# Kernel optimization log

Hardware: AMD Instinct MI355X
Metric: run time of the kernel (lower is better)

## Reference

```python
import jax, jax.numpy as jnp
import numpy as np

N_NODES = 50000
N_EDGES = 800000
IN_DIM, HID_DIM, OUT_DIM = 64, 128, 64


def gcn_conv(x, src, dst, W, b, n_nodes):
    # PyG GCNConv default: add self-loops, symmetric normalization D^-1/2 A D^-1/2
    h = x @ W  # [N, F_out]
    ones = jnp.ones(src.shape[0], dtype=x.dtype)
    deg = jax.ops.segment_sum(ones, dst, num_segments=n_nodes)  # in-degree incl. self-loops
    dinv = jnp.where(deg > 0, jax.lax.rsqrt(deg), 0.0).astype(x.dtype)
    norm = dinv[src] * dinv[dst]  # [E]
    msg = h[src] * norm[:, None]  # gather + scale, [E, F_out]
    out = jax.ops.segment_sum(msg, dst, num_segments=n_nodes)  # scatter-add
    return out + b


def setup_inputs() -> dict:
    key = jax.random.key(0)
    k1, k2, k3, k4 = jax.random.split(key, 4)
    z = jax.random.normal(k1, (N_NODES, IN_DIM), dtype=jnp.float32)
    edge_index = jax.random.randint(k2, (2, N_EDGES), 0, N_NODES, dtype=jnp.int64)
    # Glorot-style init for weights, zero bias (PyG defaults)
    W1 = jax.random.normal(k3, (IN_DIM, HID_DIM), dtype=jnp.float32) / np.sqrt(IN_DIM)
    b1 = jnp.zeros((HID_DIM,), dtype=jnp.float32)
    W2 = jax.random.normal(k4, (HID_DIM, OUT_DIM), dtype=jnp.float32) / np.sqrt(HID_DIM)
    b2 = jnp.zeros((OUT_DIM,), dtype=jnp.float32)
    return {"z": z, "edge_index": edge_index, "W1": W1, "b1": b1, "W2": W2, "b2": b2}


def reference(z, edge_index, W1, b1, W2, b2):
    n = z.shape[0]
    loops = jnp.arange(n, dtype=edge_index.dtype)
    src = jnp.concatenate([edge_index[0], loops])
    dst = jnp.concatenate([edge_index[1], loops])
    h = jax.nn.relu(gcn_conv(z, src, dst, W1, b1, n))
    x_hat = gcn_conv(h, src, dst, W2, b2, n)
    return x_hat
```

## Files before the change

### kernel.cpp

```cpp
#include <hip/hip_runtime.h>
#include <hip/hip_bf16.h>

#define N_NODES 50000
#define N_EDGES 800000
#define IN_DIM 64
#define HID_DIM 128
#define OUT_DIM 64
#define NGRP 8
#define NE8 (NGRP * N_NODES)
#define NBLK8 ((NE8 + 255) / 256)
#define MAXE 128

__device__ int g_in_f32;
__device__ int g_is64;
__device__ int g_src[N_EDGES];
__device__ int g_dst[N_EDGES];
__device__ int g_csr[N_EDGES];
__device__ int g_deg8[NE8];
__device__ int g_rowptr8[NE8 + 1];
__device__ int g_cursor8[NE8];
__device__ int g_bsum[NBLK8];
__device__ int g_boff[NBLK8];
__device__ float g_dinv[N_NODES];
__device__ __align__(16) float g_W1f[IN_DIM * HID_DIM];
__device__ __align__(16) float g_W2f[HID_DIM * OUT_DIM];
__device__ __align__(16) float g_b1f[HID_DIM];
__device__ __align__(16) float g_b2f[OUT_DIM];
__device__ __align__(16) float g_hs1[(size_t)N_NODES * HID_DIM];
__device__ __align__(16) float g_agg1[(size_t)N_NODES * HID_DIM];

__device__ __forceinline__ float loadx(const void* p, int i, int f32) {
    if (f32) return ((const float*)p)[i];
    unsigned int u = ((unsigned int)((const unsigned short*)p)[i]) << 16;
    return __uint_as_float(u);
}

__global__ void detect_kernel(const unsigned short* __restrict__ zw,
                              const unsigned int* __restrict__ ew, int E) {
    __shared__ int s_f32, s_nz;
    if (threadIdx.x == 0) { s_f32 = 0; s_nz = 0; }
    __syncthreads();
    int hit = 0;
    for (int k = 0; k < 64; k++) {
        int i = 2 * ((threadIdx.x * 64 + k) * 97);
        if (((zw[i] >> 7) & 0xFF) == 0xFF) hit = 1;
    }
    if (hit) atomicOr(&s_f32, 1);
    int nz = 0;
    int step = E / 4096;
    for (int k = 0; k < 4; k++) {
        int idx = 1 + 2 * ((threadIdx.x * 4 + k) * step);
        if (ew[idx] != 0) nz = 1;
    }
    if (nz) atomicOr(&s_nz, 1);
    __syncthreads();
    if (threadIdx.x == 0) { g_in_f32 = s_f32; g_is64 = (s_nz == 0) ? 1 : 0; }
}

__global__ void prep_kernel(const void* __restrict__ W1, const void* __restrict__ b1,
                            const void* __restrict__ W2, const void* __restrict__ b2) {
    int i = blockIdx.x * blockDim.x + threadIdx.x;
    if (i < NE8) g_deg8[i] = 0;
    int f32 = g_in_f32;
    if (i < IN_DIM * HID_DIM) g_W1f[i] = loadx(W1, i, f32);
    if (i < HID_DIM * OUT_DIM) g_W2f[i] = loadx(W2, i, f32);
    if (i < HID_DIM) g_b1f[i] = loadx(b1, i, f32);
    if (i < OUT_DIM) g_b2f[i] = loadx(b2, i, f32);
}

__global__ void convert_kernel(const void* __restrict__ ei, int N, int E) {
    int e = blockIdx.x * blockDim.x + threadIdx.x;
    if (e < E) {
        int s, d;
        if (g_is64) {
            const long long* p = (const long long*)ei;
            s = (int)p[e];
            d = (int)p[E + e];
        } else {
            const int* p = (const int*)ei;
            s = p[e];
            d = p[E + e];
        }
        g_src[e] = s;
        g_dst[e] = d;
        int g = blockIdx.x & (NGRP - 1);
        atomicAdd(&g_deg8[g * N + d], 1);
    }
}

__global__ void dinv_kernel(int N) {
    int v = blockIdx.x * blockDim.x + threadIdx.x;
    if (v < N) {
        int s = 0;
#pragma unroll
        for (int g = 0; g < NGRP; g++) s += g_deg8[g * N + v];
        g_dinv[v] = rsqrtf((float)s + 1.0f);
    }
}

__global__ __launch_bounds__(256) void localscan_kernel(int NE) {
    __shared__ int sc[256];
    int t = threadIdx.x;
    int idx = blockIdx.x * 256 + t;
    int d = (idx < NE) ? g_deg8[idx] : 0;
    sc[t] = d;
    __syncthreads();
    for (int off = 1; off < 256; off <<= 1) {
        int v = (t >= off) ? sc[t - off] : 0;
        __syncthreads();
        sc[t] += v;
        __syncthreads();
    }
    if (idx < NE) g_rowptr8[idx] = sc[t] - d;
    if (t == 255) g_bsum[blockIdx.x] = sc[255];
}

__global__ __launch_bounds__(256) void bscan_kernel(int NB, int NE, int E) {
    __shared__ int sc[256];
    int t = threadIdx.x;
    int loc[8];
    int s = 0;
#pragma unroll
    for (int j = 0; j < 8; j++) {
        int i = t * 8 + j;
        int v = (i < NB) ? g_bsum[i] : 0;
        loc[j] = s;
        s += v;
    }
    sc[t] = s;
    __syncthreads();
    for (int off = 1; off < 256; off <<= 1) {
        int v = (t >= off) ? sc[t - off] : 0;
        __syncthreads();
        sc[t] += v;
        __syncthreads();
    }
    int excl = sc[t] - s;
#pragma unroll
    for (int j = 0; j < 8; j++) {
        int i = t * 8 + j;
        if (i < NB) g_boff[i] = excl + loc[j];
    }
    if (t == 0) g_rowptr8[NE] = E;
}

__global__ __launch_bounds__(256) void addoff_kernel(int NE) {
    int idx = blockIdx.x * 256 + threadIdx.x;
    if (idx < NE) {
        int base = g_rowptr8[idx] + g_boff[blockIdx.x];
        g_rowptr8[idx] = base;
        g_cursor8[idx] = base;
    }
}

__global__ void scatter_kernel(int N, int E) {
    int e = blockIdx.x * blockDim.x + threadIdx.x;
    if (e < E) {
        int g = blockIdx.x & (NGRP - 1);
        int pos = atomicAdd(&g_cursor8[g * N + g_dst[e]], 1);
        g_csr[pos] = g_src[e];
    }
}

__global__ __launch_bounds__(256) void aggz_kernel(const void* __restrict__ z, int N) {
    __shared__ int idxbuf[4][MAXE];
    int wid = (blockIdx.x * blockDim.x + threadIdx.x) >> 6;
    if (wid >= N) return;
    int lane = threadIdx.x & 63;
    int w = threadIdx.x >> 6;
    int f32 = g_in_f32;
    int mybeg = 0, mycnt = 0;
    if (lane < NGRP) {
        mybeg = g_rowptr8[lane * N + wid];
        mycnt = g_rowptr8[lane * N + wid + 1] - mybeg;
    }
    int incl = mycnt;
#pragma unroll
    for (int off = 1; off < NGRP; off <<= 1) {
        int v = __shfl_up(incl, off, 64);
        if (lane >= off) incl += v;
    }
    int total = __shfl(incl, NGRP - 1, 64);
    int myoff = incl - mycnt;
    int* buf = idxbuf[w];
    float a0 = loadx(z, wid * IN_DIM + lane, f32) * g_dinv[wid];
    float a1 = 0.f, a2 = 0.f, a3 = 0.f, a4 = 0.f, a5 = 0.f, a6 = 0.f, a7 = 0.f;
    if (total <= MAXE) {
        if (lane < NGRP) {
            for (int i = 0; i < mycnt; i++) buf[myoff + i] = g_csr[mybeg + i];
        }
        int j = 0;
        for (; j + 8 <= total; j += 8) {
            int i0 = buf[j], i1 = buf[j+1], i2 = buf[j+2], i3 = buf[j+3];
            int i4 = buf[j+4], i5 = buf[j+5], i6 = buf[j+6], i7 = buf[j+7];
            a0 += loadx(z, i0 * IN_DIM + lane, f32) * g_dinv[i0];
            a1 += loadx(z, i1 * IN_DIM + lane, f32) * g_dinv[i1];
            a2 += loadx(z, i2 * IN_DIM + lane, f32) * g_dinv[i2];
            a3 += loadx(z, i3 * IN_DIM + lane, f32) * g_dinv[i3];
            a4 += loadx(z, i4 * IN_DIM + lane, f32) * g_dinv[i4];
            a5 += loadx(z, i5 * IN_DIM + lane, f32) * g_dinv[i5];
            a6 += loadx(z, i6 * IN_DIM + lane, f32) * g_dinv[i6];
            a7 += loadx(z, i7 * IN_DIM + lane, f32) * g_dinv[i7];
        }
        if (j + 4 <= total) {
            int i0 = buf[j], i1 = buf[j+1], i2 = buf[j+2], i3 = buf[j+3];
            a0 += loadx(z, i0 * IN_DIM + lane, f32) * g_dinv[i0];
            a1 += loadx(z, i1 * IN_DIM + lane, f32) * g_dinv[i1];
            a2 += loadx(z, i2 * IN_DIM + lane, f32) * g_dinv[i2];
            a3 += loadx(z, i3 * IN_DIM + lane, f32) * g_dinv[i3];
            j += 4;
        }
        for (; j < total; j++) {
            int i0 = buf[j];
            a0 += loadx(z, i0 * IN_DIM + lane, f32) * g_dinv[i0];
        }
    } else {
        for (int g = 0; g < NGRP; g++) {
            int beg = g_rowptr8[g * N + wid], end = g_rowptr8[g * N + wid + 1];
            for (int e = beg; e < end; e++) {
                int s = g_csr[e];
                a0 += loadx(z, s * IN_DIM + lane, f32) * g_dinv[s];
            }
        }
    }
    float acc = ((a0 + a1) + (a2 + a3)) + ((a4 + a5) + (a6 + a7));
    g_hs1[(size_t)wid * 64 + lane] = acc * g_dinv[wid];
}

__global__ __launch_bounds__(256) void gemm1_kernel(int N) {
    __shared__ float Zs[IN_DIM * 33];
    int t = threadIdx.x;
    int row0 = blockIdx.x * 32;
    const float* aggz = g_hs1;
#pragma unroll
    for (int s = 0; s < 2; s++) {
        int i = t + s * 256;
        int r = i >> 4, k4 = i & 15;
        int row = row0 + r;
        float4 v = make_float4(0.f, 0.f, 0.f, 0.f);
        if (row < N) v = *(const float4*)&aggz[(size_t)row * IN_DIM + k4 * 4];
        Zs[(k4 * 4 + 0) * 33 + r] = v.x;
        Zs[(k4 * 4 + 1) * 33 + r] = v.y;
        Zs[(k4 * 4 + 2) * 33 + r] = v.z;
        Zs[(k4 * 4 + 3) * 33 + r] = v.w;
    }
    __syncthreads();
    int cg = t & 31, rg = t >> 5;
    int c0 = cg * 4, r0 = rg * 4;
    float acc[4][4] = {};
#pragma unroll 8
    for (int k = 0; k < IN_DIM; k++) {
        float b[4];
        *(float4*)b = *(const float4*)&g_W1f[k * HID_DIM + c0];
        float a[4];
        a[0] = Zs[k * 33 + r0];
        a[1] = Zs[k * 33 + r0 + 1];
        a[2] = Zs[k * 33 + r0 + 2];
        a[3] = Zs[k * 33 + r0 + 3];
#pragma unroll
        for (int i = 0; i < 4; i++)
#pragma unroll
            for (int j = 0; j < 4; j++) acc[i][j] = fmaf(a[i], b[j], acc[i][j]);
    }
    float4 bias = *(const float4*)&g_b1f[c0];
#pragma unroll
    for (int i = 0; i < 4; i++) {
        int row = row0 + r0 + i;
        if (row < N) {
            float4 v;
            v.x = fmaxf(acc[i][0] + bias.x, 0.f);
            v.y = fmaxf(acc[i][1] + bias.y, 0.f);
            v.z = fmaxf(acc[i][2] + bias.z, 0.f);
            v.w = fmaxf(acc[i][3] + bias.w, 0.f);
            *(float4*)&g_agg1[(size_t)row * HID_DIM + c0] = v;
        }
    }
}

__global__ __launch_bounds__(256) void gemm2_kernel(int N) {
    __shared__ float Zs[64 * 33];
    int t = threadIdx.x;
    int row0 = blockIdx.x * 32;
    int cg = t & 15, rg = t >> 4;
    int c0 = cg * 4, r0 = rg * 2;
    float acc[2][4] = {};
    for (int kh = 0; kh < 2; kh++) {
        __syncthreads();
#pragma unroll
        for (int s = 0; s < 2; s++) {
            int i = t + s * 256;
            int r = i >> 4, k4 = i & 15;
            int row = row0 + r;
            float4 v = make_float4(0.f, 0.f, 0.f, 0.f);
            if (row < N) v = *(const float4*)&g_agg1[(size_t)row * HID_DIM + kh * 64 + k4 * 4];
            Zs[(k4 * 4 + 0) * 33 + r] = v.x;
            Zs[(k4 * 4 + 1) * 33 + r] = v.y;
            Zs[(k4 * 4 + 2) * 33 + r] = v.z;
            Zs[(k4 * 4 + 3) * 33 + r] = v.w;
        }
        __syncthreads();
#pragma unroll 8
        for (int k2 = 0; k2 < 64; k2++) {
            float b[4];
            *(float4*)b = *(const float4*)&g_W2f[(kh * 64 + k2) * OUT_DIM + c0];
            float a[2];
            a[0] = Zs[k2 * 33 + r0];
            a[1] = Zs[k2 * 33 + r0 + 1];
#pragma unroll
            for (int i = 0; i < 2; i++)
#pragma unroll
                for (int j = 0; j < 4; j++) acc[i][j] = fmaf(a[i], b[j], acc[i][j]);
        }
    }
#pragma unroll
    for (int i = 0; i < 2; i++) {
        int row = row0 + r0 + i;
        if (row < N) {
            float dn = g_dinv[row];
            float4 v;
            v.x = acc[i][0] * dn;
            v.y = acc[i][1] * dn;
            v.z = acc[i][2] * dn;
            v.w = acc[i][3] * dn;
            *(float4*)&g_hs1[(size_t)row * OUT_DIM + c0] = v;
        }
    }
}

__global__ __launch_bounds__(256) void agg2_kernel(void* __restrict__ out, int N) {
    __shared__ int idxbuf[4][MAXE];
    int wid = (blockIdx.x * blockDim.x + threadIdx.x) >> 6;
    if (wid >= N) return;
    int lane = threadIdx.x & 63;
    int w = threadIdx.x >> 6;
    const float* hs = g_hs1;
    int mybeg = 0, mycnt = 0;
    if (lane < NGRP) {
        mybeg = g_rowptr8[lane * N + wid];
        mycnt = g_rowptr8[lane * N + wid + 1] - mybeg;
    }
    int incl = mycnt;
#pragma unroll
    for (int off = 1; off < NGRP; off <<= 1) {
        int v = __shfl_up(incl, off, 64);
        if (lane >= off) incl += v;
    }
    int total = __shfl(incl, NGRP - 1, 64);
    int myoff = incl - mycnt;
    int* buf = idxbuf[w];
    float a0 = hs[(size_t)wid * 64 + lane];
    float a1 = 0.f, a2 = 0.f, a3 = 0.f, a4 = 0.f, a5 = 0.f, a6 = 0.f, a7 = 0.f;
    if (total <= MAXE) {
        if (lane < NGRP) {
            for (int i = 0; i < mycnt; i++) buf[myoff + i] = g_csr[mybeg + i];
        }
        int j = 0;
        for (; j + 8 <= total; j += 8) {
            int i0 = buf[j], i1 = buf[j+1], i2 = buf[j+2], i3 = buf[j+3];
            int i4 = buf[j+4], i5 = buf[j+5], i6 = buf[j+6], i7 = buf[j+7];
            a0 += hs[(size_t)i0 * 64 + lane];
            a1 += hs[(size_t)i1 * 64 + lane];
            a2 += hs[(size_t)i2 * 64 + lane];
            a3 += hs[(size_t)i3 * 64 + lane];
            a4 += hs[(size_t)i4 * 64 + lane];
            a5 += hs[(size_t)i5 * 64 + lane];
            a6 += hs[(size_t)i6 * 64 + lane];
            a7 += hs[(size_t)i7 * 64 + lane];
        }
        if (j + 4 <= total) {
            int i0 = buf[j], i1 = buf[j+1], i2 = buf[j+2], i3 = buf[j+3];
            a0 += hs[(size_t)i0 * 64 + lane];
            a1 += hs[(size_t)i1 * 64 + lane];
            a2 += hs[(size_t)i2 * 64 + lane];
            a3 += hs[(size_t)i3 * 64 + lane];
            j += 4;
        }
        for (; j < total; j++) a0 += hs[(size_t)buf[j] * 64 + lane];
    } else {
        for (int g = 0; g < NGRP; g++) {
            int beg = g_rowptr8[g * N + wid], end = g_rowptr8[g * N + wid + 1];
            for (int e = beg; e < end; e++) a0 += hs[(size_t)g_csr[e] * 64 + lane];
        }
    }
    float acc = ((a0 + a1) + (a2 + a3)) + ((a4 + a5) + (a6 + a7));
    float v = acc * g_dinv[wid] + g_b2f[lane];
    if (g_in_f32) ((float*)out)[(size_t)wid * 64 + lane] = v;
    else ((__hip_bfloat16*)out)[(size_t)wid * 64 + lane] = __float2bfloat16(v);
}

extern "C" void kernel_launch(void* const* d_in, const int* in_sizes, int n_in,
                              void* d_out, int out_size, void* d_ws, size_t ws_size,
                              hipStream_t stream) {
    const void* z  = d_in[0];
    const void* ei = d_in[1];
    const void* W1 = d_in[2];
    const void* b1 = d_in[3];
    const void* W2 = d_in[4];
    const void* b2 = d_in[5];

    const int N = in_sizes[0] / IN_DIM;
    const int E = in_sizes[1] / 2;
    const int NE = NGRP * N;

    detect_kernel<<<1, 256, 0, stream>>>((const unsigned short*)z, (const unsigned int*)ei, E);
    prep_kernel<<<NBLK8, 256, 0, stream>>>(W1, b1, W2, b2);
    convert_kernel<<<(E + 255) / 256, 256, 0, stream>>>(ei, N, E);
    dinv_kernel<<<(N + 255) / 256, 256, 0, stream>>>(N);
    localscan_kernel<<<(NE + 255) / 256, 256, 0, stream>>>(NE);
    bscan_kernel<<<1, 256, 0, stream>>>((NE + 255) / 256, NE, E);
    addoff_kernel<<<(NE + 255) / 256, 256, 0, stream>>>(NE);
    scatter_kernel<<<(E + 255) / 256, 256, 0, stream>>>(N, E);

    aggz_kernel<<<(N * 64 + 255) / 256, 256, 0, stream>>>(z, N);
    gemm1_kernel<<<(N + 31) / 32, 256, 0, stream>>>(N);
    gemm2_kernel<<<(N + 31) / 32, 256, 0, stream>>>(N);
    agg2_kernel<<<(N * 64 + 255) / 256, 256, 0, stream>>>(d_out, N);
}
```

Measured before the change: 322.3 us.

## Split feature matrices into 8-column slices for cache-friendly gather aggregation

Features are stored in eight column slices (one 32-byte chunk per node per slice), and each aggregation block now processes one slice. A wavefront handles one node, with 8 lanes per edge and 8 edges in flight, followed by a shuffle reduction. The idea is that each slice (about 1.6 MB) stays resident in cache while the random neighbour gathers run, at the cost of 8x more index-list reads and scans. A z pre-scaling kernel is added, and the GEMM loads and stores are remapped to the sliced layout.

After: 515.7 us. 60.0% more time.

```diff
diff --git a/kernel.cpp b/kernel.cpp
--- a/kernel.cpp
+++ b/kernel.cpp
@@ -9,7 +9,7 @@
 #define NGRP 8
 #define NE8 (NGRP * N_NODES)
 #define NBLK8 ((NE8 + 255) / 256)
-#define MAXE 128
+#define MAXE 256
 
 __device__ int g_in_f32;
 __device__ int g_is64;
@@ -162,13 +162,18 @@
     }
 }
 
-__global__ __launch_bounds__(256) void aggz_kernel(const void* __restrict__ z, int N) {
-    __shared__ int idxbuf[4][MAXE];
-    int wid = (blockIdx.x * blockDim.x + threadIdx.x) >> 6;
-    if (wid >= N) return;
-    int lane = threadIdx.x & 63;
-    int w = threadIdx.x >> 6;
-    int f32 = g_in_f32;
+__global__ void zprep_kernel(const void* __restrict__ z, int N) {
+    int i = blockIdx.x * blockDim.x + threadIdx.x;
+    if (i < N * IN_DIM) {
+        int node = i >> 6, c = i & 63;
+        int g = c >> 3, off = c & 7;
+        g_agg1[(size_t)g * (N * 8) + node * 8 + off] = loadx(z, i, g_in_f32) * g_dinv[node];
+    }
+}
+
+template <int SELF_SCALED>
+__device__ __forceinline__ void agg_slice(const float* __restrict__ slice, float* __restrict__ dst,
+                                          int wid, int g, int lane, int* buf, int N) {
     int mybeg = 0, mycnt = 0;
     if (lane < NGRP) {
         mybeg = g_rowptr8[lane * N + wid];
@@ -182,67 +187,67 @@
     }
     int total = __shfl(incl, NGRP - 1, 64);
     int myoff = incl - mycnt;
-    int* buf = idxbuf[w];
-    float a0 = loadx(z, wid * IN_DIM + lane, f32) * g_dinv[wid];
-    float a1 = 0.f, a2 = 0.f, a3 = 0.f, a4 = 0.f, a5 = 0.f, a6 = 0.f, a7 = 0.f;
+    int col = lane & 7;
+    int eslot = lane >> 3;
+    float acc = 0.f, acc2 = 0.f;
     if (total <= MAXE) {
         if (lane < NGRP) {
             for (int i = 0; i < mycnt; i++) buf[myoff + i] = g_csr[mybeg + i];
         }
-        int j = 0;
-        for (; j + 8 <= total; j += 8) {
-            int i0 = buf[j], i1 = buf[j+1], i2 = buf[j+2], i3 = buf[j+3];
-            int i4 = buf[j+4], i5 = buf[j+5], i6 = buf[j+6], i7 = buf[j+7];
-            a0 += loadx(z, i0 * IN_DIM + lane, f32) * g_dinv[i0];
-            a1 += loadx(z, i1 * IN_DIM + lane, f32) * g_dinv[i1];
-            a2 += loadx(z, i2 * IN_DIM + lane, f32) * g_dinv[i2];
-            a3 += loadx(z, i3 * IN_DIM + lane, f32) * g_dinv[i3];
-            a4 += loadx(z, i4 * IN_DIM + lane, f32) * g_dinv[i4];
-            a5 += loadx(z, i5 * IN_DIM + lane, f32) * g_dinv[i5];
-            a6 += loadx(z, i6 * IN_DIM + lane, f32) * g_dinv[i6];
-            a7 += loadx(z, i7 * IN_DIM + lane, f32) * g_dinv[i7];
-        }
-        if (j + 4 <= total) {
-            int i0 = buf[j], i1 = buf[j+1], i2 = buf[j+2], i3 = buf[j+3];
-            a0 += loadx(z, i0 * IN_DIM + lane, f32) * g_dinv[i0];
-            a1 += loadx(z, i1 * IN_DIM + lane, f32) * g_dinv[i1];
-            a2 += loadx(z, i2 * IN_DIM + lane, f32) * g_dinv[i2];
-            a3 += loadx(z, i3 * IN_DIM + lane, f32) * g_dinv[i3];
-            j += 4;
-        }
-        for (; j < total; j++) {
-            int i0 = buf[j];
-            a0 += loadx(z, i0 * IN_DIM + lane, f32) * g_dinv[i0];
-        }
+        int j = eslot;
+        for (; j + 8 < total; j += 16) {
+            int s0 = buf[j], s1 = buf[j + 8];
+            acc += slice[s0 * 8 + col];
+            acc2 += slice[s1 * 8 + col];
+        }
+        if (j < total) acc += slice[buf[j] * 8 + col];
     } else {
-        for (int g = 0; g < NGRP; g++) {
-            int beg = g_rowptr8[g * N + wid], end = g_rowptr8[g * N + wid + 1];
+        for (int gg = 0; gg < NGRP; gg++) {
+            int beg = g_rowptr8[gg * N + wid], end = g_rowptr8[gg * N + wid + 1];
             for (int e = beg; e < end; e++) {
                 int s = g_csr[e];
-                a0 += loadx(z, s * IN_DIM + lane, f32) * g_dinv[s];
+                if (lane < 8) acc += slice[s * 8 + col];
             }
         }
     }
-    float acc = ((a0 + a1) + (a2 + a3)) + ((a4 + a5) + (a6 + a7));
-    g_hs1[(size_t)wid * 64 + lane] = acc * g_dinv[wid];
+    acc += acc2;
+    acc += __shfl_xor(acc, 8, 64);
+    acc += __shfl_xor(acc, 16, 64);
+    acc += __shfl_xor(acc, 32, 64);
+    if (lane < 8) {
+        float v = (acc + slice[wid * 8 + col]) * g_dinv[wid];
+        dst[wid * 8 + col] = v;
+    }
+}
+
+__global__ __launch_bounds__(256) void aggz_kernel(int N) {
+    __shared__ int idxbuf[4][MAXE];
+    int g = blockIdx.x & (NGRP - 1);
+    int w = threadIdx.x >> 6;
+    int wid = (blockIdx.x >> 3) * 4 + w;
+    if (wid >= N) return;
+    int lane = threadIdx.x & 63;
+    const float* slice = g_agg1 + (size_t)g * (N * 8);
+    float* dst = g_hs1 + (size_t)g * (N * 8);
+    agg_slice<1>(slice, dst, wid, g, lane, idxbuf[w], N);
 }
 
 __global__ __launch_bounds__(256) void gemm1_kernel(int N) {
     __shared__ float Zs[IN_DIM * 33];
     int t = threadIdx.x;
     int row0 = blockIdx.x * 32;
-    const float* aggz = g_hs1;
 #pragma unroll
     for (int s = 0; s < 2; s++) {
         int i = t + s * 256;
         int r = i >> 4, k4 = i & 15;
         int row = row0 + r;
+        int g = k4 >> 1, off = (k4 & 1) * 4;
         float4 v = make_float4(0.f, 0.f, 0.f, 0.f);
-        if (row < N) v = *(const float4*)&aggz[(size_t)row * IN_DIM + k4 * 4];
-        Zs[(k4 * 4 + 0) * 33 + r] = v.x;
-        Zs[(k4 * 4 + 1) * 33 + r] = v.y;
-        Zs[(k4 * 4 + 2) * 33 + r] = v.z;
-        Zs[(k4 * 4 + 3) * 33 + r] = v.w;
+        if (row < N) v = *(const float4*)&g_hs1[(size_t)g * (N * 8) + row * 8 + off];
+        Zs[(g * 8 + off + 0) * 33 + r] = v.x;
+        Zs[(g * 8 + off + 1) * 33 + r] = v.y;
+        Zs[(g * 8 + off + 2) * 33 + r] = v.z;
+        Zs[(g * 8 + off + 3) * 33 + r] = v.w;
     }
     __syncthreads();
     int cg = t & 31, rg = t >> 5;
@@ -312,6 +317,7 @@
                 for (int j = 0; j < 4; j++) acc[i][j] = fmaf(a[i], b[j], acc[i][j]);
         }
     }
+    int gg = cg >> 1, off = (cg & 1) * 4;
 #pragma unroll
     for (int i = 0; i < 2; i++) {
         int row = row0 + r0 + i;
@@ -322,18 +328,20 @@
             v.y = acc[i][1] * dn;
             v.z = acc[i][2] * dn;
             v.w = acc[i][3] * dn;
-            *(float4*)&g_hs1[(size_t)row * OUT_DIM + c0] = v;
+            *(float4*)&g_hs1[(size_t)gg * (N * 8) + row * 8 + off] = v;
         }
     }
 }
 
 __global__ __launch_bounds__(256) void agg2_kernel(void* __restrict__ out, int N) {
     __shared__ int idxbuf[4][MAXE];
-    int wid = (blockIdx.x * blockDim.x + threadIdx.x) >> 6;
+    int g = blockIdx.x & (NGRP - 1);
+    int w = threadIdx.x >> 6;
+    int wid = (blockIdx.x >> 3) * 4 + w;
     if (wid >= N) return;
     int lane = threadIdx.x & 63;
-    int w = threadIdx.x >> 6;
-    const float* hs = g_hs1;
+    const float* slice = g_hs1 + (size_t)g * (N * 8);
+    int* buf = idxbuf[w];
     int mybeg = 0, mycnt = 0;
     if (lane < NGRP) {
         mybeg = g_rowptr8[lane * N + wid];
@@ -347,45 +355,39 @@
     }
     int total = __shfl(incl, NGRP - 1, 64);
     int myoff = incl - mycnt;
-    int* buf = idxbuf[w];
-    float a0 = hs[(size_t)wid * 64 + lane];
-    float a1 = 0.f, a2 = 0.f, a3 = 0.f, a4 = 0.f, a5 = 0.f, a6 = 0.f, a7 = 0.f;
+    int col = lane & 7;
+    int eslot = lane >> 3;
+    float acc = 0.f, acc2 = 0.f;
     if (total <= MAXE) {
         if (lane < NGRP) {
             for (int i = 0; i < mycnt; i++) buf[myoff + i] = g_csr[mybeg + i];
         }
-        int j = 0;
-        for (; j + 8 <= total; j += 8) {
-            int i0 = buf[j], i1 = buf[j+1], i2 = buf[j+2], i3 = buf[j+3];
-            int i4 = buf[j+4], i5 = buf[j+5], i6 = buf[j+6], i7 = buf[j+7];
-            a0 += hs[(size_t)i0 * 64 + lane];
-            a1 += hs[(size_t)i1 * 64 + lane];
-            a2 += hs[(size_t)i2 * 64 + lane];
-            a3 += hs[(size_t)i3 * 64 + lane];
-            a4 += hs[(size_t)i4 * 64 + lane];
-            a5 += hs[(size_t)i5 * 64 + lane];
-            a6 += hs[(size_t)i6 * 64 + lane];
-            a7 += hs[(size_t)i7 * 64 + lane];
-        }
-        if (j + 4 <= total) {
-            int i0 = buf[j], i1 = buf[j+1], i2 = buf[j+2], i3 = buf[j+3];
-            a0 += hs[(size_t)i0 * 64 + lane];
-            a1 += hs[(size_t)i1 * 64 + lane];
-            a2 += hs[(size_t)i2 * 64 + lane];
-            a3 += hs[(size_t)i3 * 64 + lane];
-            j += 4;
-        }
-        for (; j < total; j++) a0 += hs[(size_t)buf[j] * 64 + lane];
+        int j = eslot;
+        for (; j + 8 < total; j += 16) {
+            int s0 = buf[j], s1 = buf[j + 8];
+            acc += slice[s0 * 8 + col];
+            acc2 += slice[s1 * 8 + col];
+        }
+        if (j < total) acc += slice[buf[j] * 8 + col];
     } else {
-        for (int g = 0; g < NGRP; g++) {
-            int beg = g_rowptr8[g * N + wid], end = g_rowptr8[g * N + wid + 1];
-            for (int e = beg; e < end; e++) a0 += hs[(size_t)g_csr[e] * 64 + lane];
-        }
-    }
-    float acc = ((a0 + a1) + (a2 + a3)) + ((a4 + a5) + (a6 + a7));
-    float v = acc * g_dinv[wid] + g_b2f[lane];
-    if (g_in_f32) ((float*)out)[(size_t)wid * 64 + lane] = v;
-    else ((__hip_bfloat16*)out)[(size_t)wid * 64 + lane] = __float2bfloat16(v);
+        for (int gg2 = 0; gg2 < NGRP; gg2++) {
+            int beg = g_rowptr8[gg2 * N + wid], end = g_rowptr8[gg2 * N + wid + 1];
+            for (int e = beg; e < end; e++) {
+                int s = g_csr[e];
+                if (lane < 8) acc += slice[s * 8 + col];
+            }
+        }
+    }
+    acc += acc2;
+    acc += __shfl_xor(acc, 8, 64);
+    acc += __shfl_xor(acc, 16, 64);
+    acc += __shfl_xor(acc, 32, 64);
+    if (lane < 8) {
+        float v = (acc + slice[wid * 8 + col]) * g_dinv[wid] + g_b2f[g * 8 + col];
+        int oc = wid * 64 + g * 8 + col;
+        if (g_in_f32) ((float*)out)[oc] = v;
+        else ((__hip_bfloat16*)out)[oc] = __float2bfloat16(v);
+    }
 }
 
 extern "C" void kernel_launch(void* const* d_in, const int* in_sizes, int n_in,
@@ -401,6 +403,7 @@
     const int N = in_sizes[0] / IN_DIM;
     const int E = in_sizes[1] / 2;
     const int NE = NGRP * N;
+    const int aggblocks = NGRP * ((N + 3) / 4);
 
     detect_kernel<<<1, 256, 0, stream>>>((const unsigned short*)z, (const unsigned int*)ei, E);
     prep_kernel<<<NBLK8, 256, 0, stream>>>(W1, b1, W2, b2);
@@ -411,8 +414,9 @@
     addoff_kernel<<<(NE + 255) / 256, 256, 0, stream>>>(NE);
     scatter_kernel<<<(E + 255) / 256, 256, 0, stream>>>(N, E);
 
-    aggz_kernel<<<(N * 64 + 255) / 256, 256, 0, stream>>>(z, N);
+    zprep_kernel<<<(N * IN_DIM + 255) / 256, 256, 0, stream>>>(z, N);
+    aggz_kernel<<<aggblocks, 256, 0, stream>>>(N);
     gemm1_kernel<<<(N + 31) / 32, 256, 0, stream>>>(N);
     gemm2_kernel<<<(N + 31) / 32, 256, 0, stream>>>(N);
-    agg2_kernel<<<(N * 64 + 255) / 256, 256, 0, stream>>>(d_out, N);
-}
+    agg2_kernel<<<aggblocks, 256, 0, stream>>>(d_out, N);
+}
```
